# Performance work log

Measured on AMD Instinct MI355X. Metric: run time of the kernel, lower is better.

The kernel has to match this reference:

```python
import jax, jax.numpy as jnp
import numpy as np

HEADS = 16
D_MODEL = 1024
D_K = D_MODEL // HEADS


def setup_inputs() -> dict:
    key = jax.random.key(0)
    ks = jax.random.split(key, 11)
    B, S = 4, 2048
    scale = 1.0 / np.sqrt(D_MODEL)
    inp = {
        "query": jax.random.normal(ks[0], (B, S, D_MODEL), dtype=jnp.float32),
        "key": jax.random.normal(ks[1], (B, S, D_MODEL), dtype=jnp.float32),
        "value": jax.random.normal(ks[2], (B, S, D_MODEL), dtype=jnp.float32),
        "Wq": jax.random.normal(ks[3], (D_MODEL, D_MODEL), dtype=jnp.float32) * scale,
        "bq": jnp.zeros((D_MODEL,), dtype=jnp.float32),
        "Wk": jax.random.normal(ks[4], (D_MODEL, D_MODEL), dtype=jnp.float32) * scale,
        "bk": jnp.zeros((D_MODEL,), dtype=jnp.float32),
        "Wv": jax.random.normal(ks[5], (D_MODEL, D_MODEL), dtype=jnp.float32) * scale,
        "bv": jnp.zeros((D_MODEL,), dtype=jnp.float32),
        "Wo": jax.random.normal(ks[6], (D_MODEL, D_MODEL), dtype=jnp.float32) * scale,
        "bo": jnp.zeros((D_MODEL,), dtype=jnp.float32),
    }
    return inp


def reference(query, key, value, Wq, bq, Wk, bk, Wv, bv, Wo, bo):
    B, S, _ = query.shape
    # Linear projections, split into heads: [B,S,D] -> [B,H,S,d_k]
    def proj(x, W, b):
        y = x @ W.T + b
        return y.reshape(B, S, HEADS, D_K).transpose(0, 2, 1, 3)

    q = proj(query, Wq, bq)
    k = proj(key, Wk, bk)
    v = proj(value, Wv, bv)

    scores = jnp.einsum("bhqd,bhkd->bhqk", q, k) / jnp.sqrt(jnp.float32(D_K))
    p_attn = jax.nn.softmax(scores, axis=-1)  # dropout is identity in eval
    x = jnp.einsum("bhqk,bhkd->bhqd", p_attn, v)
    x = x.transpose(0, 2, 1, 3).reshape(B, S, HEADS * D_K)
    return x @ Wo.T + bo
```

## Files before the change

kernel.cpp:

```cpp
#include <hip/hip_runtime.h>
#include <hip/hip_bf16.h>
#include <stdint.h>

#define D_MODEL 1024
#define HEADS   16
#define DK      64
#define BATCH   4
#define SEQ     2048
#define MROWS   (BATCH * SEQ)

typedef __attribute__((ext_vector_type(8))) short bf16x8;
typedef __attribute__((ext_vector_type(4))) float f32x4;
typedef __attribute__((ext_vector_type(4))) unsigned int u32x4;
typedef __attribute__((ext_vector_type(2))) unsigned int u32x2;

#define SCQ 0.18033688011112042f

__device__ __forceinline__ unsigned pk2bf(float a, float b) {
  __hip_bfloat162 h = __float22bfloat162_rn(float2{a, b});
  union { __hip_bfloat162 h; unsigned u; } c; c.h = h;
  return c.u;
}
__device__ __forceinline__ unsigned short n2bf(float f) {
  __hip_bfloat16 h = __float2bfloat16(f);
  union { __hip_bfloat16 h; unsigned short s; } c; c.h = h;
  return c.s;
}

__device__ __forceinline__ int swz64(int row, int col) {
  return row * 64 + (col ^ ((row & 7) << 3));
}

__global__ __launch_bounds__(256) void cvt4(const float* __restrict__ w0, const float* __restrict__ w1,
                                            const float* __restrict__ w2, const float* __restrict__ w3,
                                            unsigned short* __restrict__ o0, unsigned short* __restrict__ o1,
                                            unsigned short* __restrict__ o2, unsigned short* __restrict__ o3) {
  const int which = blockIdx.x >> 10;
  const float* in; unsigned short* out;
  if (which == 0)      { in = w0; out = o0; }
  else if (which == 1) { in = w1; out = o1; }
  else if (which == 2) { in = w2; out = o2; }
  else                 { in = w3; out = o3; }
  const int i = ((blockIdx.x & 1023) * 256 + threadIdx.x) * 4;
  f32x4 v = *(const f32x4*)(in + i);
  u32x2 w;
  w[0] = pk2bf(v[0], v[1]);
  w[1] = pk2bf(v[2], v[3]);
  *(u32x2*)(out + i) = w;
}

__global__ __launch_bounds__(256) void qkv_gemm(const float* __restrict__ Aq, const float* __restrict__ Ak,
                                                const float* __restrict__ Av,
                                                const unsigned short* __restrict__ Bq,
                                                const unsigned short* __restrict__ Bk,
                                                const unsigned short* __restrict__ Bv,
                                                const float* __restrict__ bq_, const float* __restrict__ bk_,
                                                const float* __restrict__ bv_,
                                                unsigned short* __restrict__ Qo, unsigned short* __restrict__ Ko,
                                                unsigned short* __restrict__ Vo) {
  __shared__ unsigned short As[2][128 * 40];
  __shared__ unsigned short Bs[2][128 * 40];

  const int which = blockIdx.x >> 9;
  const int bx = blockIdx.x & 511;
  const float* Af = which == 0 ? Aq : which == 1 ? Ak : Av;
  const unsigned short* Bw = which == 0 ? Bq : which == 1 ? Bk : Bv;
  const float* bias = which == 0 ? bq_ : which == 1 ? bk_ : bv_;

  const int tid = threadIdx.x;
  const int lane = tid & 63, wid = tid >> 6;
  const int l16 = lane & 15, lg = lane >> 4;
  const int wrow = (wid >> 1) * 64, wcol = (wid & 1) * 64;

  const int swzb = (bx & 7) * 64 + (bx >> 3);
  const int m0 = (swzb >> 3) * 128, n0 = (swzb & 7) * 128;

  const int sr2 = tid >> 1, sc16 = (tid & 1) * 16;
  const float* aSrc = Af + (size_t)(m0 + sr2) * D_MODEL + sc16;
  const unsigned short* bSrc = Bw + (size_t)(n0 + sr2) * D_MODEL + sc16;

  f32x4 acc[4][4];
  const f32x4 zero = {0.f, 0.f, 0.f, 0.f};
#pragma unroll
  for (int i = 0; i < 4; ++i)
#pragma unroll
    for (int j = 0; j < 4; ++j) acc[i][j] = zero;

  f32x4 a0 = *(const f32x4*)aSrc, a1 = *(const f32x4*)(aSrc + 4),
        a2 = *(const f32x4*)(aSrc + 8), a3 = *(const f32x4*)(aSrc + 12);
  u32x4 br0 = *(const u32x4*)bSrc, br1 = *(const u32x4*)(bSrc + 8);

#pragma unroll 1
  for (int kt = 0; kt < D_MODEL / 32; ++kt) {
    const int buf = kt & 1;
    u32x4 pa, pb;
    pa[0] = pk2bf(a0[0], a0[1]); pa[1] = pk2bf(a0[2], a0[3]);
    pa[2] = pk2bf(a1[0], a1[1]); pa[3] = pk2bf(a1[2], a1[3]);
    pb[0] = pk2bf(a2[0], a2[1]); pb[1] = pk2bf(a2[2], a2[3]);
    pb[2] = pk2bf(a3[0], a3[1]); pb[3] = pk2bf(a3[2], a3[3]);
    *(u32x4*)&As[buf][sr2 * 40 + sc16] = pa;
    *(u32x4*)&As[buf][sr2 * 40 + sc16 + 8] = pb;
    *(u32x4*)&Bs[buf][sr2 * 40 + sc16] = br0;
    *(u32x4*)&Bs[buf][sr2 * 40 + sc16 + 8] = br1;
    __syncthreads();
    if (kt + 1 < D_MODEL / 32) {
      const float* an = aSrc + (kt + 1) * 32;
      a0 = *(const f32x4*)an; a1 = *(const f32x4*)(an + 4);
      a2 = *(const f32x4*)(an + 8); a3 = *(const f32x4*)(an + 12);
      const unsigned short* bn = bSrc + (kt + 1) * 32;
      br0 = *(const u32x4*)bn; br1 = *(const u32x4*)(bn + 8);
    }

    bf16x8 af[4], bfr[4];
#pragma unroll
    for (int i = 0; i < 4; ++i) {
      af[i]  = *(const bf16x8*)&As[buf][(wrow + i * 16 + l16) * 40 + lg * 8];
      bfr[i] = *(const bf16x8*)&Bs[buf][(wcol + i * 16 + l16) * 40 + lg * 8];
    }
#pragma unroll
    for (int i = 0; i < 4; ++i)
#pragma unroll
      for (int j = 0; j < 4; ++j)
        acc[i][j] = __builtin_amdgcn_mfma_f32_16x16x32_bf16(af[i], bfr[j], acc[i][j], 0, 0, 0);
  }

  const float scale = (which == 0) ? SCQ : 1.0f;
#pragma unroll
  for (int j = 0; j < 4; ++j) {
    const int col = n0 + wcol + j * 16 + l16;
    const float bv = bias[col];
    if (which == 2) {
      const int hh = col >> 6, dd = col & 63;
#pragma unroll
      for (int i = 0; i < 4; ++i) {
        const int row0 = m0 + wrow + i * 16 + lg * 4;
        u32x2 pw;
        pw[0] = pk2bf(acc[i][j][0] + bv, acc[i][j][1] + bv);
        pw[1] = pk2bf(acc[i][j][2] + bv, acc[i][j][3] + bv);
        unsigned short* dst = Vo +
            ((((size_t)(row0 >> 11) * HEADS + hh) * DK + dd) * SEQ + (row0 & (SEQ - 1)));
        *(u32x2*)dst = pw;
      }
    } else {
      unsigned short* Outp = which == 0 ? Qo : Ko;
#pragma unroll
      for (int i = 0; i < 4; ++i) {
        const int row0 = m0 + wrow + i * 16 + lg * 4;
#pragma unroll
        for (int r = 0; r < 4; ++r)
          Outp[(size_t)(row0 + r) * D_MODEL + col] = n2bf((acc[i][j][r] + bv) * scale);
      }
    }
  }
}

__global__ __launch_bounds__(256) void out_gemm(const unsigned short* __restrict__ Ab,
                                                const unsigned short* __restrict__ Bw,
                                                const float* __restrict__ bias,
                                                float* __restrict__ Outp) {
  __shared__ unsigned short As[2][128 * 40];
  __shared__ unsigned short Bs[2][128 * 40];

  const int tid = threadIdx.x;
  const int lane = tid & 63, wid = tid >> 6;
  const int l16 = lane & 15, lg = lane >> 4;
  const int wrow = (wid >> 1) * 64, wcol = (wid & 1) * 64;

  const int bx = blockIdx.x;
  const int swzb = (bx & 7) * 64 + (bx >> 3);
  const int m0 = (swzb >> 3) * 128, n0 = (swzb & 7) * 128;

  const int sr2 = tid >> 1, sc16 = (tid & 1) * 16;
  const unsigned short* aSrc = Ab + (size_t)(m0 + sr2) * D_MODEL + sc16;
  const unsigned short* bSrc = Bw + (size_t)(n0 + sr2) * D_MODEL + sc16;

  f32x4 acc[4][4];
  const f32x4 zero = {0.f, 0.f, 0.f, 0.f};
#pragma unroll
  for (int i = 0; i < 4; ++i)
#pragma unroll
    for (int j = 0; j < 4; ++j) acc[i][j] = zero;

  u32x4 ar0 = *(const u32x4*)aSrc, ar1 = *(const u32x4*)(aSrc + 8);
  u32x4 br0 = *(const u32x4*)bSrc, br1 = *(const u32x4*)(bSrc + 8);

#pragma unroll 1
  for (int kt = 0; kt < D_MODEL / 32; ++kt) {
    const int buf = kt & 1;
    *(u32x4*)&As[buf][sr2 * 40 + sc16] = ar0;
    *(u32x4*)&As[buf][sr2 * 40 + sc16 + 8] = ar1;
    *(u32x4*)&Bs[buf][sr2 * 40 + sc16] = br0;
    *(u32x4*)&Bs[buf][sr2 * 40 + sc16 + 8] = br1;
    __syncthreads();
    if (kt + 1 < D_MODEL / 32) {
      const unsigned short* an = aSrc + (kt + 1) * 32;
      ar0 = *(const u32x4*)an; ar1 = *(const u32x4*)(an + 8);
      const unsigned short* bn = bSrc + (kt + 1) * 32;
      br0 = *(const u32x4*)bn; br1 = *(const u32x4*)(bn + 8);
    }

    bf16x8 af[4], bfr[4];
#pragma unroll
    for (int i = 0; i < 4; ++i) {
      af[i]  = *(const bf16x8*)&As[buf][(wrow + i * 16 + l16) * 40 + lg * 8];
      bfr[i] = *(const bf16x8*)&Bs[buf][(wcol + i * 16 + l16) * 40 + lg * 8];
    }
#pragma unroll
    for (int i = 0; i < 4; ++i)
#pragma unroll
      for (int j = 0; j < 4; ++j)
        acc[i][j] = __builtin_amdgcn_mfma_f32_16x16x32_bf16(af[i], bfr[j], acc[i][j], 0, 0, 0);
  }

#pragma unroll
  for (int j = 0; j < 4; ++j) {
    const int col = n0 + wcol + j * 16 + l16;
    const float bv = bias[col];
#pragma unroll
    for (int i = 0; i < 4; ++i) {
      const int row0 = m0 + wrow + i * 16 + lg * 4;
#pragma unroll
      for (int r = 0; r < 4; ++r)
        Outp[(size_t)(row0 + r) * D_MODEL + col] = acc[i][j][r] + bv;
    }
  }
}

__global__ __launch_bounds__(256, 2) void attn_v10(const unsigned short* __restrict__ Qb,
                                                   const unsigned short* __restrict__ Kb,
                                                   const unsigned short* __restrict__ Vtg,
                                                   unsigned short* __restrict__ Xo) {
  __shared__ unsigned short Ks[2][64 * 64];
  __shared__ unsigned short Vt[2][64 * 64];
  __shared__ unsigned short Ps[4][64 * 64];

  const int tid = threadIdx.x;
  const int lane = tid & 63, w = tid >> 6;
  const int l16 = lane & 15, lg = lane >> 4;

  const int p = blockIdx.x;
  const int lb = (p & 7) * 64 + (p >> 3);
  const int qb = lb & 7, bh = lb >> 3;
  const int b = bh >> 4, h = bh & 15;

  const size_t srow0 = (size_t)b * SEQ + qb * 256;
  const unsigned short* Qp = Qb + srow0 * D_MODEL + h * DK;
  const unsigned short* Kp = Kb + (size_t)b * SEQ * D_MODEL + h * DK;
  const unsigned short* Vp = Vtg + (size_t)bh * DK * SEQ;

  const int sr = tid >> 2;
  const int scol = (tid & 3) * 16;

  bf16x8 qfrag[4][2];
#pragma unroll
  for (int qf = 0; qf < 4; ++qf)
#pragma unroll
    for (int kh = 0; kh < 2; ++kh)
      qfrag[qf][kh] = *(const bf16x8*)(Qp + (size_t)(w * 64 + qf * 16 + l16) * D_MODEL + kh * 32 + lg * 8);

  u32x4 kr0, kr1, vr0, vr1;
  {
    const unsigned short* ksrc = Kp + (size_t)sr * D_MODEL + scol;
    kr0 = *(const u32x4*)ksrc; kr1 = *(const u32x4*)(ksrc + 8);
    const unsigned short* vsrc = Vp + (size_t)sr * SEQ + scol;
    vr0 = *(const u32x4*)vsrc; vr1 = *(const u32x4*)(vsrc + 8);
  }

  float lsum[4];
  f32x4 acco[4][4];
  const f32x4 zero = {0.f, 0.f, 0.f, 0.f};
#pragma unroll
  for (int qf = 0; qf < 4; ++qf) {
    lsum[qf] = 0.f;
#pragma unroll
    for (int df = 0; df < 4; ++df) acco[qf][df] = zero;
  }

  unsigned short* Psw = Ps[w];
  const int srcbase = (lane & 48) | ((lane & 48) >> 2);

#pragma unroll 1
  for (int kb = 0; kb < SEQ / 64; ++kb) {
    const int buf = kb & 1;
    *(u32x4*)&Ks[buf][swz64(sr, scol)] = kr0;
    *(u32x4*)&Ks[buf][swz64(sr, scol + 8)] = kr1;
    *(u32x4*)&Vt[buf][swz64(sr, scol)] = vr0;
    *(u32x4*)&Vt[buf][swz64(sr, scol + 8)] = vr1;
    __syncthreads();
    if (kb + 1 < SEQ / 64) {
      const unsigned short* ksrc = Kp + (size_t)((kb + 1) * 64 + sr) * D_MODEL + scol;
      kr0 = *(const u32x4*)ksrc; kr1 = *(const u32x4*)(ksrc + 8);
      const unsigned short* vsrc = Vp + (size_t)sr * SEQ + (kb + 1) * 64 + scol;
      vr0 = *(const u32x4*)vsrc; vr1 = *(const u32x4*)(vsrc + 8);
    }

    f32x4 sc[4][4];
#pragma unroll
    for (int qf = 0; qf < 4; ++qf)
#pragma unroll
      for (int tf = 0; tf < 4; ++tf) sc[qf][tf] = zero;
#pragma unroll
    for (int tf = 0; tf < 4; ++tf) {
      bf16x8 k0 = *(const bf16x8*)&Ks[buf][swz64(tf * 16 + l16, lg * 8)];
      bf16x8 k1 = *(const bf16x8*)&Ks[buf][swz64(tf * 16 + l16, 32 + lg * 8)];
#pragma unroll
      for (int qf = 0; qf < 4; ++qf) {
        sc[qf][tf] = __builtin_amdgcn_mfma_f32_16x16x32_bf16(k0, qfrag[qf][0], sc[qf][tf], 0, 0, 0);
        sc[qf][tf] = __builtin_amdgcn_mfma_f32_16x16x32_bf16(k1, qfrag[qf][1], sc[qf][tf], 0, 0, 0);
      }
    }

#pragma unroll
    for (int qf = 0; qf < 4; ++qf) {
      float sum = 0.f;
#pragma unroll
      for (int tf = 0; tf < 4; ++tf)
#pragma unroll
        for (int r = 0; r < 4; ++r) {
          const float pv = __builtin_amdgcn_exp2f(sc[qf][tf][r]);
          sc[qf][tf][r] = pv;
          sum += pv;
        }
      lsum[qf] += sum;
#pragma unroll
      for (int tf = 0; tf < 4; ++tf) {
        u32x2 pw;
        pw[0] = pk2bf(sc[qf][tf][0], sc[qf][tf][1]);
        pw[1] = pk2bf(sc[qf][tf][2], sc[qf][tf][3]);
        *(u32x2*)&Psw[swz64(qf * 16 + l16, tf * 16 + lg * 4)] = pw;
      }
    }

    bf16x8 pf[4][2];
#pragma unroll
    for (int qf = 0; qf < 4; ++qf)
#pragma unroll
      for (int k2 = 0; k2 < 2; ++k2)
        pf[qf][k2] = *(const bf16x8*)&Psw[swz64(qf * 16 + l16, k2 * 32 + lg * 8)];

#pragma unroll
    for (int df = 0; df < 4; ++df) {
      bf16x8 v0 = *(const bf16x8*)&Vt[buf][swz64(df * 16 + l16, lg * 8)];
      bf16x8 v1 = *(const bf16x8*)&Vt[buf][swz64(df * 16 + l16, 32 + lg * 8)];
#pragma unroll
      for (int qf = 0; qf < 4; ++qf) {
        acco[qf][df] = __builtin_amdgcn_mfma_f32_16x16x32_bf16(pf[qf][0], v0, acco[qf][df], 0, 0, 0);
        acco[qf][df] = __builtin_amdgcn_mfma_f32_16x16x32_bf16(pf[qf][1], v1, acco[qf][df], 0, 0, 0);
      }
    }
  }

#pragma unroll
  for (int qf = 0; qf < 4; ++qf) {
    lsum[qf] += __shfl_xor(lsum[qf], 16);
    lsum[qf] += __shfl_xor(lsum[qf], 32);
  }

  unsigned short* dst = Xo + (srow0 + w * 64) * D_MODEL + h * DK;
#pragma unroll
  for (int qf = 0; qf < 4; ++qf) {
    const float inv = 1.f / lsum[qf];
#pragma unroll
    for (int r = 0; r < 4; ++r) {
      const float rr = __shfl(inv, srcbase + r);
      const int row = qf * 16 + lg * 4 + r;
#pragma unroll
      for (int df = 0; df < 4; ++df)
        dst[(size_t)row * D_MODEL + df * 16 + l16] = n2bf(acco[qf][df][r] * rr);
    }
  }
}

extern "C" void kernel_launch(void* const* d_in, const int* in_sizes, int n_in,
                              void* d_out, int out_size, void* d_ws, size_t ws_size,
                              hipStream_t stream) {
  const float* query = (const float*)d_in[0];
  const float* key_  = (const float*)d_in[1];
  const float* value = (const float*)d_in[2];
  const float* Wq = (const float*)d_in[3];
  const float* bq = (const float*)d_in[4];
  const float* Wk = (const float*)d_in[5];
  const float* bk = (const float*)d_in[6];
  const float* Wv = (const float*)d_in[7];
  const float* bv = (const float*)d_in[8];
  const float* Wo = (const float*)d_in[9];
  const float* bo = (const float*)d_in[10];

  unsigned short* ws  = (unsigned short*)d_ws;
  unsigned short* WqB = ws;
  unsigned short* WkB = WqB + (1u << 20);
  unsigned short* WvB = WkB + (1u << 20);
  unsigned short* WoB = WvB + (1u << 20);
  unsigned short* Qb  = WoB + (1u << 20);
  unsigned short* Kb  = Qb + (size_t)MROWS * D_MODEL;
  unsigned short* Vtg = Kb + (size_t)MROWS * D_MODEL;
  unsigned short* Xb  = Vtg + (size_t)MROWS * D_MODEL;
  if (ws_size < (size_t)(4u * (1u << 20) + 4u * (size_t)MROWS * D_MODEL) * 2u) return;

  cvt4<<<4096, 256, 0, stream>>>(Wq, Wk, Wv, Wo, WqB, WkB, WvB, WoB);

  qkv_gemm<<<1536, 256, 0, stream>>>(query, key_, value, WqB, WkB, WvB, bq, bk, bv, Qb, Kb, Vtg);

  attn_v10<<<512, 256, 0, stream>>>(Qb, Kb, Vtg, Xb);

  out_gemm<<<512, 256, 0, stream>>>(Xb, WoB, bo, (float*)d_out);
}
```

Baseline: 207.7 us.

## Rewrite attention with 32x32 MFMA, register-resident P, and direct global-to-LDS loads

```diff
diff --git a/kernel.cpp b/kernel.cpp
--- a/kernel.cpp
+++ b/kernel.cpp
@@ -11,6 +11,7 @@
 
 typedef __attribute__((ext_vector_type(8))) short bf16x8;
 typedef __attribute__((ext_vector_type(4))) float f32x4;
+typedef __attribute__((ext_vector_type(16))) float f32x16;
 typedef __attribute__((ext_vector_type(4))) unsigned int u32x4;
 typedef __attribute__((ext_vector_type(2))) unsigned int u32x2;
 
@@ -27,8 +28,10 @@
   return c.s;
 }
 
-__device__ __forceinline__ int swz64(int row, int col) {
-  return row * 64 + (col ^ ((row & 7) << 3));
+__device__ __forceinline__ void gl_lds16(const void* g, void* l) {
+  __builtin_amdgcn_global_load_lds(
+      (const __attribute__((address_space(1))) unsigned int*)g,
+      (__attribute__((address_space(3))) unsigned int*)l, 16, 0, 0);
 }
 
 __global__ __launch_bounds__(256) void cvt4(const float* __restrict__ w0, const float* __restrict__ w1,
@@ -226,148 +229,126 @@
   }
 }
 
-__global__ __launch_bounds__(256, 2) void attn_v10(const unsigned short* __restrict__ Qb,
+__global__ __launch_bounds__(256, 4) void attn_v11(const unsigned short* __restrict__ Qb,
                                                    const unsigned short* __restrict__ Kb,
                                                    const unsigned short* __restrict__ Vtg,
                                                    unsigned short* __restrict__ Xo) {
-  __shared__ unsigned short Ks[2][64 * 64];
-  __shared__ unsigned short Vt[2][64 * 64];
-  __shared__ unsigned short Ps[4][64 * 64];
+  __shared__ unsigned short Ks[2][32 * 128];
+  __shared__ unsigned short Vt[2][32 * 128];
+  __shared__ float Lbuf[4][32];
 
   const int tid = threadIdx.x;
   const int lane = tid & 63, w = tid >> 6;
-  const int l16 = lane & 15, lg = lane >> 4;
+  const int l32 = lane & 31, hi = lane >> 5;
+  const int rsel = l32 >> 1;
+  const int xorm = rsel << 3;
+  const int cbase = (l32 & 1) * 64 + hi * 8;
 
   const int p = blockIdx.x;
-  const int lb = (p & 7) * 64 + (p >> 3);
-  const int qb = lb & 7, bh = lb >> 3;
+  const int lb = (p & 7) * 128 + (p >> 3);
+  const int qb = lb & 15, bh = lb >> 4;
   const int b = bh >> 4, h = bh & 15;
 
-  const size_t srow0 = (size_t)b * SEQ + qb * 256;
+  const size_t srow0 = (size_t)b * SEQ + qb * 128;
   const unsigned short* Qp = Qb + srow0 * D_MODEL + h * DK;
   const unsigned short* Kp = Kb + (size_t)b * SEQ * D_MODEL + h * DK;
   const unsigned short* Vp = Vtg + (size_t)bh * DK * SEQ;
 
-  const int sr = tid >> 2;
-  const int scol = (tid & 3) * 16;
-
-  bf16x8 qfrag[4][2];
-#pragma unroll
-  for (int qf = 0; qf < 4; ++qf)
-#pragma unroll
-    for (int kh = 0; kh < 2; ++kh)
-      qfrag[qf][kh] = *(const bf16x8*)(Qp + (size_t)(w * 64 + qf * 16 + l16) * D_MODEL + kh * 32 + lg * 8);
-
-  u32x4 kr0, kr1, vr0, vr1;
-  {
-    const unsigned short* ksrc = Kp + (size_t)sr * D_MODEL + scol;
-    kr0 = *(const u32x4*)ksrc; kr1 = *(const u32x4*)(ksrc + 8);
-    const unsigned short* vsrc = Vp + (size_t)sr * SEQ + scol;
-    vr0 = *(const u32x4*)vsrc; vr1 = *(const u32x4*)(vsrc + 8);
-  }
-
-  float lsum[4];
-  f32x4 acco[4][4];
-  const f32x4 zero = {0.f, 0.f, 0.f, 0.f};
-#pragma unroll
-  for (int qf = 0; qf < 4; ++qf) {
-    lsum[qf] = 0.f;
-#pragma unroll
-    for (int df = 0; df < 4; ++df) acco[qf][df] = zero;
-  }
-
-  unsigned short* Psw = Ps[w];
-  const int srcbase = (lane & 48) | ((lane & 48) >> 2);
+  bf16x8 qfrag[4];
+#pragma unroll
+  for (int s = 0; s < 4; ++s)
+    qfrag[s] = *(const bf16x8*)(Qp + (size_t)(w * 32 + l32) * D_MODEL + s * 16 + hi * 8);
+
+  const unsigned short* kSrc[2];
+  const unsigned short* vSrc[2];
+  int ldsByte[2];
+#pragma unroll
+  for (int c = 0; c < 2; ++c) {
+    const int eo = (tid + c * 256) * 8;
+    const int rp = eo >> 7;
+    const int cl = (eo & 127) ^ ((rp & 15) << 3);
+    const int tr = rp * 2 + (cl >> 6);
+    const int cc = cl & 63;
+    kSrc[c] = Kp + (size_t)tr * D_MODEL + cc;
+    vSrc[c] = Vp + (size_t)tr * SEQ + cc;
+    ldsByte[c] = (tid + c * 256) * 16;
+  }
+
+#pragma unroll
+  for (int c = 0; c < 2; ++c) {
+    gl_lds16(kSrc[c], (char*)Ks[0] + ldsByte[c]);
+    gl_lds16(vSrc[c], (char*)Vt[0] + ldsByte[c]);
+  }
+
+  f32x16 acc[2];
+#pragma unroll
+  for (int i = 0; i < 16; ++i) { acc[0][i] = 0.f; acc[1][i] = 0.f; }
+  float lsum = 0.f;
 
 #pragma unroll 1
   for (int kb = 0; kb < SEQ / 64; ++kb) {
     const int buf = kb & 1;
-    *(u32x4*)&Ks[buf][swz64(sr, scol)] = kr0;
-    *(u32x4*)&Ks[buf][swz64(sr, scol + 8)] = kr1;
-    *(u32x4*)&Vt[buf][swz64(sr, scol)] = vr0;
-    *(u32x4*)&Vt[buf][swz64(sr, scol + 8)] = vr1;
     __syncthreads();
     if (kb + 1 < SEQ / 64) {
-      const unsigned short* ksrc = Kp + (size_t)((kb + 1) * 64 + sr) * D_MODEL + scol;
-      kr0 = *(const u32x4*)ksrc; kr1 = *(const u32x4*)(ksrc + 8);
-      const unsigned short* vsrc = Vp + (size_t)sr * SEQ + (kb + 1) * 64 + scol;
-      vr0 = *(const u32x4*)vsrc; vr1 = *(const u32x4*)(vsrc + 8);
-    }
-
-    f32x4 sc[4][4];
-#pragma unroll
-    for (int qf = 0; qf < 4; ++qf)
-#pragma unroll
-      for (int tf = 0; tf < 4; ++tf) sc[qf][tf] = zero;
-#pragma unroll
-    for (int tf = 0; tf < 4; ++tf) {
-      bf16x8 k0 = *(const bf16x8*)&Ks[buf][swz64(tf * 16 + l16, lg * 8)];
-      bf16x8 k1 = *(const bf16x8*)&Ks[buf][swz64(tf * 16 + l16, 32 + lg * 8)];
-#pragma unroll
-      for (int qf = 0; qf < 4; ++qf) {
-        sc[qf][tf] = __builtin_amdgcn_mfma_f32_16x16x32_bf16(k0, qfrag[qf][0], sc[qf][tf], 0, 0, 0);
-        sc[qf][tf] = __builtin_amdgcn_mfma_f32_16x16x32_bf16(k1, qfrag[qf][1], sc[qf][tf], 0, 0, 0);
-      }
-    }
-
-#pragma unroll
-    for (int qf = 0; qf < 4; ++qf) {
-      float sum = 0.f;
-#pragma unroll
-      for (int tf = 0; tf < 4; ++tf)
-#pragma unroll
-        for (int r = 0; r < 4; ++r) {
-          const float pv = __builtin_amdgcn_exp2f(sc[qf][tf][r]);
-          sc[qf][tf][r] = pv;
-          sum += pv;
+#pragma unroll
+      for (int c = 0; c < 2; ++c) {
+        gl_lds16(kSrc[c] + (size_t)(kb + 1) * 64 * D_MODEL, (char*)Ks[buf ^ 1] + ldsByte[c]);
+        gl_lds16(vSrc[c] + (size_t)(kb + 1) * 64, (char*)Vt[buf ^ 1] + ldsByte[c]);
+      }
+    }
+
+#pragma unroll
+    for (int tt = 0; tt < 2; ++tt) {
+      f32x16 d;
+#pragma unroll
+      for (int i = 0; i < 16; ++i) d[i] = 0.f;
+#pragma unroll
+      for (int s = 0; s < 4; ++s) {
+        bf16x8 kf = *(const bf16x8*)&Ks[buf][(tt * 16 + rsel) * 128 + ((cbase + s * 16) ^ xorm)];
+        d = __builtin_amdgcn_mfma_f32_32x32x16_bf16(kf, qfrag[s], d, 0, 0, 0);
+      }
+
+      unsigned pk[4][2];
+#pragma unroll
+      for (int g = 0; g < 4; ++g) {
+        const float e0 = __builtin_amdgcn_exp2f(d[g * 4 + 0]);
+        const float e1 = __builtin_amdgcn_exp2f(d[g * 4 + 1]);
+        const float e2 = __builtin_amdgcn_exp2f(d[g * 4 + 2]);
+        const float e3 = __builtin_amdgcn_exp2f(d[g * 4 + 3]);
+        lsum += (e0 + e1) + (e2 + e3);
+        pk[g][0] = pk2bf(e0, e1);
+        pk[g][1] = pk2bf(e2, e3);
+      }
+
+#pragma unroll
+      for (int s2 = 0; s2 < 2; ++s2) {
+        unsigned a0 = pk[2 * s2][0], b0 = pk[2 * s2 + 1][0];
+        unsigned a1 = pk[2 * s2][1], b1 = pk[2 * s2 + 1][1];
+        asm("v_permlane32_swap_b32 %0, %1" : "+v"(a0), "+v"(b0));
+        asm("v_permlane32_swap_b32 %0, %1" : "+v"(a1), "+v"(b1));
+        union { unsigned u[4]; bf16x8 v; } pf;
+        pf.u[0] = a0; pf.u[1] = a1; pf.u[2] = b0; pf.u[3] = b1;
+        const int tcol = tt * 32 + s2 * 16;
+#pragma unroll
+        for (int dt = 0; dt < 2; ++dt) {
+          bf16x8 vf = *(const bf16x8*)&Vt[buf][(dt * 16 + rsel) * 128 + ((cbase + tcol) ^ xorm)];
+          acc[dt] = __builtin_amdgcn_mfma_f32_32x32x16_bf16(pf.v, vf, acc[dt], 0, 0, 0);
         }
-      lsum[qf] += sum;
-#pragma unroll
-      for (int tf = 0; tf < 4; ++tf) {
-        u32x2 pw;
-        pw[0] = pk2bf(sc[qf][tf][0], sc[qf][tf][1]);
-        pw[1] = pk2bf(sc[qf][tf][2], sc[qf][tf][3]);
-        *(u32x2*)&Psw[swz64(qf * 16 + l16, tf * 16 + lg * 4)] = pw;
-      }
-    }
-
-    bf16x8 pf[4][2];
-#pragma unroll
-    for (int qf = 0; qf < 4; ++qf)
-#pragma unroll
-      for (int k2 = 0; k2 < 2; ++k2)
-        pf[qf][k2] = *(const bf16x8*)&Psw[swz64(qf * 16 + l16, k2 * 32 + lg * 8)];
-
-#pragma unroll
-    for (int df = 0; df < 4; ++df) {
-      bf16x8 v0 = *(const bf16x8*)&Vt[buf][swz64(df * 16 + l16, lg * 8)];
-      bf16x8 v1 = *(const bf16x8*)&Vt[buf][swz64(df * 16 + l16, 32 + lg * 8)];
-#pragma unroll
-      for (int qf = 0; qf < 4; ++qf) {
-        acco[qf][df] = __builtin_amdgcn_mfma_f32_16x16x32_bf16(pf[qf][0], v0, acco[qf][df], 0, 0, 0);
-        acco[qf][df] = __builtin_amdgcn_mfma_f32_16x16x32_bf16(pf[qf][1], v1, acco[qf][df], 0, 0, 0);
-      }
-    }
-  }
-
-#pragma unroll
-  for (int qf = 0; qf < 4; ++qf) {
-    lsum[qf] += __shfl_xor(lsum[qf], 16);
-    lsum[qf] += __shfl_xor(lsum[qf], 32);
-  }
-
-  unsigned short* dst = Xo + (srow0 + w * 64) * D_MODEL + h * DK;
-#pragma unroll
-  for (int qf = 0; qf < 4; ++qf) {
-    const float inv = 1.f / lsum[qf];
-#pragma unroll
-    for (int r = 0; r < 4; ++r) {
-      const float rr = __shfl(inv, srcbase + r);
-      const int row = qf * 16 + lg * 4 + r;
-#pragma unroll
-      for (int df = 0; df < 4; ++df)
-        dst[(size_t)row * D_MODEL + df * 16 + l16] = n2bf(acco[qf][df][r] * rr);
-    }
+      }
+    }
+  }
+
+  lsum += __shfl_xor(lsum, 32);
+  if (hi == 0) Lbuf[w][l32] = lsum;
+
+  unsigned short* dst = Xo + (srow0 + w * 32) * D_MODEL + h * DK;
+#pragma unroll
+  for (int reg = 0; reg < 16; ++reg) {
+    const int q = (reg & 3) + 8 * (reg >> 2) + 4 * hi;
+    const float inv = 1.f / Lbuf[w][q];
+#pragma unroll
+    for (int dt = 0; dt < 2; ++dt)
+      dst[(size_t)q * D_MODEL + dt * 32 + l32] = n2bf(acc[dt][reg] * inv);
   }
 }
 
@@ -401,7 +382,7 @@
 
   qkv_gemm<<<1536, 256, 0, stream>>>(query, key_, value, WqB, WkB, WvB, bq, bk, bv, Qb, Kb, Vtg);
 
-  attn_v10<<<512, 256, 0, stream>>>(Qb, Kb, Vtg, Xb);
+  attn_v11<<<1024, 256, 0, stream>>>(Qb, Kb, Vtg, Xb);
 
   out_gemm<<<512, 256, 0, stream>>>(Xb, WoB, bo, (float*)d_out);
 }
```

Measured after the change: 215.7 us. 3.9% more time.
